# Kernel tuning notes

Hardware: AMD Instinct MI355X
Metric: run time of the kernel (lower is better)

Reference implementation:

```python
import jax, jax.numpy as jnp
import numpy as np

N_NODES = 100000
N_EDGES = 600000
IN_C, HID_C, OUT_C = 128, 128, 64


def gcn_conv(x, W, b, src, dst, n_nodes):
    """PyG GCNConv: out = D^{-1/2} (A + I) D^{-1/2} X W + b (symmetric norm, self-loops)."""
    h = x @ W  # [N, C_out] transform first (as PyG does)
    # add self loops
    loop = jnp.arange(n_nodes, dtype=src.dtype)
    s = jnp.concatenate([src, loop])
    d = jnp.concatenate([dst, loop])
    # degree over targets (edge weight = 1)
    deg = jax.ops.segment_sum(jnp.ones_like(d, dtype=h.dtype), d, num_segments=n_nodes)
    dinv = jnp.where(deg > 0, jax.lax.rsqrt(deg), 0.0)
    norm = dinv[s] * dinv[d]  # [E+N]
    msg = h[s] * norm[:, None]  # gather + scale
    out = jax.ops.segment_sum(msg, d, num_segments=n_nodes)  # scatter-add
    return out + b


def setup_inputs() -> dict:
    key = jax.random.key(0)
    k1, k2, k3, k4, k5 = jax.random.split(key, 5)
    x = jax.random.normal(k1, (N_NODES, IN_C), dtype=jnp.float32)
    src = jax.random.randint(k2, (N_EDGES,), 0, N_NODES, dtype=jnp.int32)
    dst = jax.random.randint(k3, (N_EDGES,), 0, N_NODES, dtype=jnp.int32)
    # Glorot-style init for conv weights, zero bias (PyG defaults)
    W1 = jax.random.normal(k4, (IN_C, HID_C), dtype=jnp.float32) * (1.0 / np.sqrt(IN_C))
    W2 = jax.random.normal(k5, (HID_C, OUT_C), dtype=jnp.float32) * (1.0 / np.sqrt(HID_C))
    b1 = jnp.zeros((HID_C,), dtype=jnp.float32)
    b2 = jnp.zeros((OUT_C,), dtype=jnp.float32)
    return {"x": x, "W1": W1, "b1": b1, "W2": W2, "b2": b2, "src": src, "dst": dst}


def reference(x, W1, b1, W2, b2, src, dst):
    h = gcn_conv(x, W1, b1, src, dst, N_NODES)
    h = jax.nn.relu(h)
    out = gcn_conv(h, W2, b2, src, dst, N_NODES)
    return out
```

## Files before the change

### kernel.cpp

```cpp
#include <hip/hip_runtime.h>
#include <math.h>


typedef __bf16 bf16x8 __attribute__((ext_vector_type(8)));
typedef float f32x4 __attribute__((ext_vector_type(4)));

union ABu {
  unsigned short u16[8];
  uint4 u4;
  bf16x8 v;
};

__device__ inline unsigned short f2bf(float f) {
  unsigned u = __float_as_uint(f);
  return (unsigned short)((u + 0x7fffu + ((u >> 16) & 1u)) >> 16);
}

__device__ inline void unpack8(uint4 v, float* f) {
  f[0] = __uint_as_float(v.x << 16);
  f[1] = __uint_as_float(v.x & 0xffff0000u);
  f[2] = __uint_as_float(v.y << 16);
  f[3] = __uint_as_float(v.y & 0xffff0000u);
  f[4] = __uint_as_float(v.z << 16);
  f[5] = __uint_as_float(v.z & 0xffff0000u);
  f[6] = __uint_as_float(v.w << 16);
  f[7] = __uint_as_float(v.w & 0xffff0000u);
}

__device__ inline uint4 pack8(const float* a) {
  uint4 o;
  o.x = (unsigned)f2bf(a[0]) | ((unsigned)f2bf(a[1]) << 16);
  o.y = (unsigned)f2bf(a[2]) | ((unsigned)f2bf(a[3]) << 16);
  o.z = (unsigned)f2bf(a[4]) | ((unsigned)f2bf(a[5]) << 16);
  o.w = (unsigned)f2bf(a[6]) | ((unsigned)f2bf(a[7]) << 16);
  return o;
}

constexpr int SCAN_CHUNK = 1024;

__global__ __launch_bounds__(256) void k_pre(const float* __restrict__ W1,
                                             const float* __restrict__ W2,
                                             unsigned short* __restrict__ Wb1,
                                             unsigned short* __restrict__ Wb2,
                                             int* __restrict__ counts, int n) {
  constexpr int CONV_BLOCKS = (128 * 128 + 128 * 64) / 256;
  if (blockIdx.x < CONV_BLOCKS) {
    int idx = blockIdx.x * 256 + threadIdx.x;
    if (idx < 128 * 128) {
      int k = idx >> 7, c = idx & 127;
      Wb1[(((k >> 3) << 7) + c) * 8 + (k & 7)] = f2bf(W1[idx]);
    } else {
      int j = idx - 128 * 128;
      int k = j >> 6, c = j & 63;
      Wb2[(((k >> 3) << 6) + c) * 8 + (k & 7)] = f2bf(W2[j]);
    }
    return;
  }
  int i = (blockIdx.x - CONV_BLOCKS) * 256 + threadIdx.x;
  if (i < n) counts[i] = 0;
}

__global__ __launch_bounds__(256) void k_count_rank(const int* __restrict__ dst,
                                                    int* __restrict__ counts,
                                                    int* __restrict__ rank, int E) {
  int base = (blockIdx.x * 256 + threadIdx.x) * 4;
  if (base + 3 < E) {
    int4 d = *(const int4*)(dst + base);
    int4 r;
    r.x = atomicAdd(&counts[d.x], 1);
    r.y = atomicAdd(&counts[d.y], 1);
    r.z = atomicAdd(&counts[d.z], 1);
    r.w = atomicAdd(&counts[d.w], 1);
    *(int4*)(rank + base) = r;
  } else {
    for (int e = base; e < E; ++e) rank[e] = atomicAdd(&counts[dst[e]], 1);
  }
}

__global__ __launch_bounds__(256) void k_scan1(const int* __restrict__ counts,
                                               int* __restrict__ offsets,
                                               int* __restrict__ aux,
                                               float* __restrict__ dinv, int n) {
  __shared__ int tsum[256];
  int tid = threadIdx.x;
  int base = blockIdx.x * SCAN_CHUNK + tid * 4;
  int v0 = (base + 0 < n) ? counts[base + 0] : 0;
  int v1 = (base + 1 < n) ? counts[base + 1] : 0;
  int v2 = (base + 2 < n) ? counts[base + 2] : 0;
  int v3 = (base + 3 < n) ? counts[base + 3] : 0;
  int s = v0 + v1 + v2 + v3;
  tsum[tid] = s;
  __syncthreads();
  for (int off = 1; off < 256; off <<= 1) {
    int t = (tid >= off) ? tsum[tid - off] : 0;
    __syncthreads();
    tsum[tid] += t;
    __syncthreads();
  }
  int excl = tsum[tid] - s;
  if (base + 0 < n) { offsets[base + 0] = excl;              dinv[base + 0] = rsqrtf((float)(v0 + 1)); }
  if (base + 1 < n) { offsets[base + 1] = excl + v0;         dinv[base + 1] = rsqrtf((float)(v1 + 1)); }
  if (base + 2 < n) { offsets[base + 2] = excl + v0 + v1;    dinv[base + 2] = rsqrtf((float)(v2 + 1)); }
  if (base + 3 < n) { offsets[base + 3] = excl + v0 + v1 + v2; dinv[base + 3] = rsqrtf((float)(v3 + 1)); }
  if (tid == 255) aux[blockIdx.x] = tsum[255];
}

__global__ __launch_bounds__(256) void k_scan3(int* __restrict__ offsets,
                                               const int* __restrict__ aux,
                                               int n, int E, int G) {
  __shared__ int saux[256];
  int tid = threadIdx.x;
  int v = (tid < G) ? aux[tid] : 0;
  saux[tid] = v;
  __syncthreads();
  for (int off = 1; off < 256; off <<= 1) {
    int t = (tid >= off) ? saux[tid - off] : 0;
    __syncthreads();
    saux[tid] += t;
    __syncthreads();
  }
  int excl = saux[tid] - v;
  __syncthreads();
  saux[tid] = excl;
  __syncthreads();

  int i = blockIdx.x * 256 + tid;
  if (i < n) offsets[i] += saux[i >> 10];
  if (i == 0) offsets[n] = E;
}

__global__ __launch_bounds__(256) void k_scatter(const int* __restrict__ src,
                                                 const int* __restrict__ dst,
                                                 const int* __restrict__ offsets,
                                                 const int* __restrict__ rank,
                                                 int* __restrict__ esrc, int E) {
  int base = (blockIdx.x * 256 + threadIdx.x) * 4;
  if (base + 3 < E) {
    int4 s = *(const int4*)(src + base);
    int4 d = *(const int4*)(dst + base);
    int4 r = *(const int4*)(rank + base);
    esrc[offsets[d.x] + r.x] = s.x;
    esrc[offsets[d.y] + r.y] = s.y;
    esrc[offsets[d.z] + r.z] = s.z;
    esrc[offsets[d.w] + r.w] = s.w;
  } else {
    for (int e = base; e < E; ++e) esrc[offsets[dst[e]] + rank[e]] = src[e];
  }
}

__global__ __launch_bounds__(256) void k_gemm1(const float* __restrict__ X,
                                               const unsigned short* __restrict__ Wb,
                                               const float* __restrict__ dinv,
                                               unsigned short* __restrict__ Cb, int M) {
  constexpr int K = 128, N = 128, NT = N / 16, KS = K / 32;
  const int tid = threadIdx.x;
  const int wave = tid >> 6;
  const int lane = tid & 63;
  const int q = lane >> 4;
  const int l15 = lane & 15;
  const int row0 = blockIdx.x * 64 + wave * 16;
  const int rowA = row0 + l15;

  f32x4 zero = {0.0f, 0.0f, 0.0f, 0.0f};
  f32x4 acc[NT];
#pragma unroll
  for (int t = 0; t < NT; ++t) acc[t] = zero;

#pragma unroll
  for (int kk = 0; kk < KS; ++kk) {
    ABu a;
    float4 f0 = make_float4(0.f, 0.f, 0.f, 0.f);
    float4 f1 = make_float4(0.f, 0.f, 0.f, 0.f);
    if (rowA < M) {
      const float4* ap = (const float4*)(X + (size_t)rowA * K + kk * 32 + q * 8);
      f0 = ap[0];
      f1 = ap[1];
    }
    a.u16[0] = f2bf(f0.x); a.u16[1] = f2bf(f0.y);
    a.u16[2] = f2bf(f0.z); a.u16[3] = f2bf(f0.w);
    a.u16[4] = f2bf(f1.x); a.u16[5] = f2bf(f1.y);
    a.u16[6] = f2bf(f1.z); a.u16[7] = f2bf(f1.w);
#pragma unroll
    for (int nt = 0; nt < NT; ++nt) {
      ABu b;
      b.u4 = *(const uint4*)(Wb + ((size_t)(kk * 4 + q) * N + nt * 16 + l15) * 8);
      acc[nt] = __builtin_amdgcn_mfma_f32_16x16x32_bf16(a.v, b.v, acc[nt], 0, 0, 0);
    }
  }

#pragma unroll
  for (int v = 0; v < 4; ++v) {
    int row = row0 + q * 4 + v;
    if (row < M) {
      float di = dinv[row];
#pragma unroll
      for (int nt = 0; nt < NT; ++nt)
        Cb[(size_t)row * N + nt * 16 + l15] = f2bf(acc[nt][v] * di);
    }
  }
}

__global__ __launch_bounds__(256) void k_aggemm(const unsigned short* __restrict__ h1s,
                                                const float* __restrict__ dinv,
                                                const float* __restrict__ b1,
                                                const int* __restrict__ offsets,
                                                const int* __restrict__ esrc,
                                                const unsigned short* __restrict__ Wb2,
                                                unsigned short* __restrict__ h2s,
                                                int n) {
  constexpr int LDA = 136;
  __shared__ unsigned short As[16 * LDA];
  __shared__ float sdinv[16];
  const int tid = threadIdx.x;

  {
    const int nl = tid >> 4;
    const int q = tid & 15;
    const int node = blockIdx.x * 16 + nl;
    float acc[8];
    if (node < n) {
      const uint4* h4 = (const uint4*)h1s;
      float di = dinv[node];
      if (q == 0) sdinv[nl] = di;
      unpack8(h4[(size_t)node * 16 + q], acc);
      int e0 = offsets[node];
      int e1 = offsets[node + 1];
      for (int e = e0; e < e1; e += 8) {
        int idx[8];
#pragma unroll
        for (int i = 0; i < 8; ++i) {
          int ee = e + i < e1 ? e + i : e1 - 1;
          idx[i] = esrc[ee];
        }
        uint4 rr[8];
#pragma unroll
        for (int i = 0; i < 8; ++i) rr[i] = h4[(size_t)idx[i] * 16 + q];
#pragma unroll
        for (int i = 0; i < 8; ++i) {
          float w = (e + i < e1) ? 1.f : 0.f;
          float g[8];
          unpack8(rr[i], g);
#pragma unroll
          for (int j = 0; j < 8; ++j) acc[j] = fmaf(g[j], w, acc[j]);
        }
      }
      const float4* b14 = (const float4*)b1;
      float4 ba = b14[q * 2], bb = b14[q * 2 + 1];
      float bias[8] = {ba.x, ba.y, ba.z, ba.w, bb.x, bb.y, bb.z, bb.w};
#pragma unroll
      for (int i = 0; i < 8; ++i) acc[i] = fmaxf(fmaf(acc[i], di, bias[i]), 0.f);
    } else {
      if (q == 0) sdinv[nl] = 0.f;
#pragma unroll
      for (int i = 0; i < 8; ++i) acc[i] = 0.f;
    }
    *(uint4*)&As[nl * LDA + q * 8] = pack8(acc);
  }
  __syncthreads();

  {
    const int wave = tid >> 6;
    const int lane = tid & 63;
    const int q = lane >> 4;
    const int l15 = lane & 15;
    f32x4 acc = {0.0f, 0.0f, 0.0f, 0.0f};
#pragma unroll
    for (int kk = 0; kk < 4; ++kk) {
      ABu a, b;
      a.u4 = *(const uint4*)&As[l15 * LDA + kk * 32 + q * 8];
      b.u4 = *(const uint4*)(Wb2 + ((size_t)(kk * 4 + q) * 64 + wave * 16 + l15) * 8);
      acc = __builtin_amdgcn_mfma_f32_16x16x32_bf16(a.v, b.v, acc, 0, 0, 0);
    }
#pragma unroll
    for (int v = 0; v < 4; ++v) {
      int rl = q * 4 + v;
      int row = blockIdx.x * 16 + rl;
      if (row < n) h2s[(size_t)row * 64 + wave * 16 + l15] = f2bf(acc[v] * sdinv[rl]);
    }
  }
}

__global__ __launch_bounds__(256) void k_agg2(const unsigned short* __restrict__ h2s,
                                              const float* __restrict__ dinv,
                                              const float* __restrict__ b2,
                                              const int* __restrict__ offsets,
                                              const int* __restrict__ esrc,
                                              float* __restrict__ out, int n) {
  constexpr int CQ = 8;
  const int tid = threadIdx.x;
  const int node = blockIdx.x * 32 + tid / CQ;
  const int q = tid % CQ;
  if (node >= n) return;

  const uint4* h4 = (const uint4*)h2s;
  float di = dinv[node];
  float acc[8];
  unpack8(h4[(size_t)node * CQ + q], acc);

  int e0 = offsets[node];
  int e1 = offsets[node + 1];
  for (int e = e0; e < e1; e += 8) {
    int idx[8];
#pragma unroll
    for (int i = 0; i < 8; ++i) {
      int ee = e + i < e1 ? e + i : e1 - 1;
      idx[i] = esrc[ee];
    }
    uint4 rr[8];
#pragma unroll
    for (int i = 0; i < 8; ++i) rr[i] = h4[(size_t)idx[i] * CQ + q];
#pragma unroll
    for (int i = 0; i < 8; ++i) {
      float w = (e + i < e1) ? 1.f : 0.f;
      float g[8];
      unpack8(rr[i], g);
#pragma unroll
      for (int j = 0; j < 8; ++j) acc[j] = fmaf(g[j], w, acc[j]);
    }
  }

  const float4* b24 = (const float4*)b2;
  float4 ba = b24[q * 2], bb = b24[q * 2 + 1];
  float bias[8] = {ba.x, ba.y, ba.z, ba.w, bb.x, bb.y, bb.z, bb.w};
  float4 o0, o1;
  o0.x = fmaf(acc[0], di, bias[0]);
  o0.y = fmaf(acc[1], di, bias[1]);
  o0.z = fmaf(acc[2], di, bias[2]);
  o0.w = fmaf(acc[3], di, bias[3]);
  o1.x = fmaf(acc[4], di, bias[4]);
  o1.y = fmaf(acc[5], di, bias[5]);
  o1.z = fmaf(acc[6], di, bias[6]);
  o1.w = fmaf(acc[7], di, bias[7]);
  ((float4*)out)[(size_t)node * 16 + q * 2 + 0] = o0;
  ((float4*)out)[(size_t)node * 16 + q * 2 + 1] = o1;
}


extern "C" void kernel_launch(void* const* d_in, const int* in_sizes, int n_in,
                              void* d_out, int out_size, void* d_ws, size_t ws_size,
                              hipStream_t stream) {
  const float* x  = (const float*)d_in[0];
  const float* W1 = (const float*)d_in[1];
  const float* b1 = (const float*)d_in[2];
  const float* W2 = (const float*)d_in[3];
  const float* b2 = (const float*)d_in[4];
  const int* src  = (const int*)d_in[5];
  const int* dst  = (const int*)d_in[6];
  float* out = (float*)d_out;

  constexpr int IN_C = 128, HID_C = 128, OUT_C = 64;
  const int N = in_sizes[0] / IN_C;
  const int E = in_sizes[5];

  char* p = (char*)d_ws;
  auto alloc = [&](size_t bytes) {
    char* r = p;
    p += (bytes + 255) & ~(size_t)255;
    return r;
  };
  float* dinv    = (float*)alloc((size_t)N * 4);
  int*   offsets = (int*)alloc((size_t)(N + 1) * 4);
  int*   counts  = (int*)alloc((size_t)N * 4);
  int*   rank    = (int*)alloc((size_t)E * 4);
  int*   aux     = (int*)alloc(1024);
  int*   esrc    = (int*)alloc((size_t)E * 4);
  unsigned short* Wb1 = (unsigned short*)alloc((size_t)IN_C * HID_C * 2);
  unsigned short* Wb2 = (unsigned short*)alloc((size_t)HID_C * OUT_C * 2);
  unsigned short* h1s = (unsigned short*)alloc((size_t)N * HID_C * 2);
  unsigned short* h2s = (unsigned short*)alloc((size_t)N * OUT_C * 2);

  const int T = 256;
  const int G = (N + SCAN_CHUNK - 1) / SCAN_CHUNK;
  const int E4B = ((E + 3) / 4 + T - 1) / T;
  constexpr int CONV_BLOCKS = (128 * 128 + 128 * 64) / 256;

  k_pre<<<CONV_BLOCKS + (N + T - 1) / T, T, 0, stream>>>(W1, W2, Wb1, Wb2, counts, N);
  k_count_rank<<<E4B, T, 0, stream>>>(dst, counts, rank, E);
  k_scan1<<<G, T, 0, stream>>>(counts, offsets, aux, dinv, N);
  k_scan3<<<(N + T - 1) / T, T, 0, stream>>>(offsets, aux, N, E, G);
  k_scatter<<<E4B, T, 0, stream>>>(src, dst, offsets, rank, esrc, E);
  k_gemm1<<<(N + 63) / 64, T, 0, stream>>>(x, Wb1, dinv, h1s, N);
  k_aggemm<<<(N + 15) / 16, T, 0, stream>>>(h1s, dinv, b1, offsets, esrc, Wb2, h2s, N);
  k_agg2<<<(N + 31) / 32, T, 0, stream>>>(h2s, dinv, b2, offsets, esrc, out, N);
}
```

Measured before the change: 211.2 us.

## Privatize degree counters into block-group copies to reduce atomic contention

Degree counting now writes to NG=8 separate counter arrays, picked by block index modulo 8, so atomics from different block groups land on different addresses. The scan sums the 8 copies per node and builds a per-group base offset array. The scatter uses that array so each edge still gets a unique CSR slot. This should cut contention on the counting atomics, but the counter arrays and the zeroing, scan and fixup passes become eight times larger, adding memory traffic.

```diff
diff --git a/kernel.cpp b/kernel.cpp
--- a/kernel.cpp
+++ b/kernel.cpp
@@ -4,6 +4,8 @@
 
 typedef __bf16 bf16x8 __attribute__((ext_vector_type(8)));
 typedef float f32x4 __attribute__((ext_vector_type(4)));
+
+constexpr int NG = 8;
 
 union ABu {
   unsigned short u16[8];
@@ -42,7 +44,7 @@
                                              const float* __restrict__ W2,
                                              unsigned short* __restrict__ Wb1,
                                              unsigned short* __restrict__ Wb2,
-                                             int* __restrict__ counts, int n) {
+                                             int* __restrict__ counts, int n8) {
   constexpr int CONV_BLOCKS = (128 * 128 + 128 * 64) / 256;
   if (blockIdx.x < CONV_BLOCKS) {
     int idx = blockIdx.x * 256 + threadIdx.x;
@@ -57,38 +59,56 @@
     return;
   }
   int i = (blockIdx.x - CONV_BLOCKS) * 256 + threadIdx.x;
-  if (i < n) counts[i] = 0;
+  if (i < n8) counts[i] = 0;
 }
 
 __global__ __launch_bounds__(256) void k_count_rank(const int* __restrict__ dst,
                                                     int* __restrict__ counts,
-                                                    int* __restrict__ rank, int E) {
+                                                    int* __restrict__ rank,
+                                                    int E, int N) {
+  int* cnt = counts + (size_t)(blockIdx.x & (NG - 1)) * N;
   int base = (blockIdx.x * 256 + threadIdx.x) * 4;
   if (base + 3 < E) {
     int4 d = *(const int4*)(dst + base);
     int4 r;
-    r.x = atomicAdd(&counts[d.x], 1);
-    r.y = atomicAdd(&counts[d.y], 1);
-    r.z = atomicAdd(&counts[d.z], 1);
-    r.w = atomicAdd(&counts[d.w], 1);
+    r.x = atomicAdd(&cnt[d.x], 1);
+    r.y = atomicAdd(&cnt[d.y], 1);
+    r.z = atomicAdd(&cnt[d.z], 1);
+    r.w = atomicAdd(&cnt[d.w], 1);
     *(int4*)(rank + base) = r;
   } else {
-    for (int e = base; e < E; ++e) rank[e] = atomicAdd(&counts[dst[e]], 1);
+    for (int e = base; e < E; ++e) rank[e] = atomicAdd(&cnt[dst[e]], 1);
   }
 }
 
 __global__ __launch_bounds__(256) void k_scan1(const int* __restrict__ counts,
                                                int* __restrict__ offsets,
+                                               int* __restrict__ gbase,
                                                int* __restrict__ aux,
                                                float* __restrict__ dinv, int n) {
   __shared__ int tsum[256];
   int tid = threadIdx.x;
   int base = blockIdx.x * SCAN_CHUNK + tid * 4;
-  int v0 = (base + 0 < n) ? counts[base + 0] : 0;
-  int v1 = (base + 1 < n) ? counts[base + 1] : 0;
-  int v2 = (base + 2 < n) ? counts[base + 2] : 0;
-  int v3 = (base + 3 < n) ? counts[base + 3] : 0;
-  int s = v0 + v1 + v2 + v3;
+
+  int tot[4];
+  int pre[4][NG];
+#pragma unroll
+  for (int j = 0; j < 4; ++j) {
+    int i = base + j;
+    int t = 0;
+    if (i < n) {
+#pragma unroll
+      for (int g = 0; g < NG; ++g) {
+        pre[j][g] = t;
+        t += counts[(size_t)g * n + i];
+      }
+    } else {
+#pragma unroll
+      for (int g = 0; g < NG; ++g) pre[j][g] = 0;
+    }
+    tot[j] = t;
+  }
+  int s = tot[0] + tot[1] + tot[2] + tot[3];
   tsum[tid] = s;
   __syncthreads();
   for (int off = 1; off < 256; off <<= 1) {
@@ -98,14 +118,24 @@
     __syncthreads();
   }
   int excl = tsum[tid] - s;
-  if (base + 0 < n) { offsets[base + 0] = excl;              dinv[base + 0] = rsqrtf((float)(v0 + 1)); }
-  if (base + 1 < n) { offsets[base + 1] = excl + v0;         dinv[base + 1] = rsqrtf((float)(v1 + 1)); }
-  if (base + 2 < n) { offsets[base + 2] = excl + v0 + v1;    dinv[base + 2] = rsqrtf((float)(v2 + 1)); }
-  if (base + 3 < n) { offsets[base + 3] = excl + v0 + v1 + v2; dinv[base + 3] = rsqrtf((float)(v3 + 1)); }
+
+  int run = excl;
+#pragma unroll
+  for (int j = 0; j < 4; ++j) {
+    int i = base + j;
+    if (i < n) {
+      offsets[i] = run;
+      dinv[i] = rsqrtf((float)(tot[j] + 1));
+#pragma unroll
+      for (int g = 0; g < NG; ++g) gbase[(size_t)g * n + i] = run + pre[j][g];
+      run += tot[j];
+    }
+  }
   if (tid == 255) aux[blockIdx.x] = tsum[255];
 }
 
 __global__ __launch_bounds__(256) void k_scan3(int* __restrict__ offsets,
+                                               int* __restrict__ gbase,
                                                const int* __restrict__ aux,
                                                int n, int E, int G) {
   __shared__ int saux[256];
@@ -125,26 +155,32 @@
   __syncthreads();
 
   int i = blockIdx.x * 256 + tid;
-  if (i < n) offsets[i] += saux[i >> 10];
+  if (i < n) {
+    int fix = saux[i >> 10];
+    offsets[i] += fix;
+#pragma unroll
+    for (int g = 0; g < NG; ++g) gbase[(size_t)g * n + i] += fix;
+  }
   if (i == 0) offsets[n] = E;
 }
 
 __global__ __launch_bounds__(256) void k_scatter(const int* __restrict__ src,
                                                  const int* __restrict__ dst,
-                                                 const int* __restrict__ offsets,
+                                                 const int* __restrict__ gbase,
                                                  const int* __restrict__ rank,
-                                                 int* __restrict__ esrc, int E) {
+                                                 int* __restrict__ esrc, int E, int N) {
+  const int* gb = gbase + (size_t)(blockIdx.x & (NG - 1)) * N;
   int base = (blockIdx.x * 256 + threadIdx.x) * 4;
   if (base + 3 < E) {
     int4 s = *(const int4*)(src + base);
     int4 d = *(const int4*)(dst + base);
     int4 r = *(const int4*)(rank + base);
-    esrc[offsets[d.x] + r.x] = s.x;
-    esrc[offsets[d.y] + r.y] = s.y;
-    esrc[offsets[d.z] + r.z] = s.z;
-    esrc[offsets[d.w] + r.w] = s.w;
+    esrc[gb[d.x] + r.x] = s.x;
+    esrc[gb[d.y] + r.y] = s.y;
+    esrc[gb[d.z] + r.z] = s.z;
+    esrc[gb[d.w] + r.w] = s.w;
   } else {
-    for (int e = base; e < E; ++e) esrc[offsets[dst[e]] + rank[e]] = src[e];
+    for (int e = base; e < E; ++e) esrc[gb[dst[e]] + rank[e]] = src[e];
   }
 }
 
@@ -360,7 +396,8 @@
   };
   float* dinv    = (float*)alloc((size_t)N * 4);
   int*   offsets = (int*)alloc((size_t)(N + 1) * 4);
-  int*   counts  = (int*)alloc((size_t)N * 4);
+  int*   counts  = (int*)alloc((size_t)NG * N * 4);
+  int*   gbase   = (int*)alloc((size_t)NG * N * 4);
   int*   rank    = (int*)alloc((size_t)E * 4);
   int*   aux     = (int*)alloc(1024);
   int*   esrc    = (int*)alloc((size_t)E * 4);
@@ -374,11 +411,12 @@
   const int E4B = ((E + 3) / 4 + T - 1) / T;
   constexpr int CONV_BLOCKS = (128 * 128 + 128 * 64) / 256;
 
-  k_pre<<<CONV_BLOCKS + (N + T - 1) / T, T, 0, stream>>>(W1, W2, Wb1, Wb2, counts, N);
-  k_count_rank<<<E4B, T, 0, stream>>>(dst, counts, rank, E);
-  k_scan1<<<G, T, 0, stream>>>(counts, offsets, aux, dinv, N);
-  k_scan3<<<(N + T - 1) / T, T, 0, stream>>>(offsets, aux, N, E, G);
-  k_scatter<<<E4B, T, 0, stream>>>(src, dst, offsets, rank, esrc, E);
+  k_pre<<<CONV_BLOCKS + (NG * N + T - 1) / T, T, 0, stream>>>(W1, W2, Wb1, Wb2,
+                                                              counts, NG * N);
+  k_count_rank<<<E4B, T, 0, stream>>>(dst, counts, rank, E, N);
+  k_scan1<<<G, T, 0, stream>>>(counts, offsets, gbase, aux, dinv, N);
+  k_scan3<<<(N + T - 1) / T, T, 0, stream>>>(offsets, gbase, aux, N, E, G);
+  k_scatter<<<E4B, T, 0, stream>>>(src, dst, gbase, rank, esrc, E, N);
   k_gemm1<<<(N + 63) / 64, T, 0, stream>>>(x, Wb1, dinv, h1s, N);
   k_aggemm<<<(N + 15) / 16, T, 0, stream>>>(h1s, dinv, b1, offsets, esrc, Wb2, h2s, N);
   k_agg2<<<(N + 31) / 32, T, 0, stream>>>(h2s, dinv, b2, offsets, esrc, out, N);
```

After: 216.0 us. 2.3% more time.
